# Optimization experiments

Hardware: AMD Instinct MI355X
Metric: run time of the kernel (lower is better)

Reference implementation:

```python
import jax, jax.numpy as jnp
import numpy as np

B, N, C = 64, 512, 1280


def setup_inputs() -> dict:
    key = jax.random.key(0)
    ks = jax.random.split(key, 10)
    scale = 0.02
    x = jax.random.normal(ks[0], (B, N, C), dtype=jnp.float32)
    Mask = jax.random.randint(ks[1], (B, N, N), 0, 2, dtype=jnp.int32)
    Wq = jax.random.normal(ks[2], (C, C), dtype=jnp.float32) * scale
    bq = jnp.zeros((C,), dtype=jnp.float32)
    Wk = jax.random.normal(ks[3], (C, C), dtype=jnp.float32) * scale
    bk = jnp.zeros((C,), dtype=jnp.float32)
    Wv = jax.random.normal(ks[4], (C, C), dtype=jnp.float32) * scale
    bv = jnp.zeros((C,), dtype=jnp.float32)
    Wr = jax.random.normal(ks[5], (C, C), dtype=jnp.float32) * scale
    br = jnp.zeros((C,), dtype=jnp.float32)
    return {"x": x, "Mask": Mask, "Wq": Wq, "bq": bq, "Wk": Wk, "bk": bk,
            "Wv": Wv, "bv": bv, "Wr": Wr, "br": br}


def reference(x, Mask, Wq, bq, Wk, bk, Wv, bv, Wr, br):
    # q, k, v: [B, N, C]
    q = x @ Wq + bq
    k = x @ Wk + bk
    v = x @ Wv + bv
    # scores[b, n, m] = q[b, n] . k[b, m]  -> [B, N, N]
    scores = jnp.einsum('bnc,bmc->bnm', q, k)
    # masked_fill BEFORE the scale divide, as in the original module
    scores = jnp.where(Mask == 0, jnp.float32(-1e20), scores)
    attn = jax.nn.softmax(scores / jnp.sqrt(jnp.float32(C)), axis=-1)
    # original: (V^T @ attn).permute -> out[b, n, c] = sum_m v[b, m, c] * attn[b, m, n]
    att_feat = jnp.einsum('bmc,bmn->bnc', v, attn)
    return att_feat @ Wr + br
```

## Files before the change

kernel.cpp:

```cpp
#include <hip/hip_runtime.h>
#include <hip/hip_bf16.h>

#define DI __device__ __forceinline__

typedef __attribute__((ext_vector_type(8))) short short8;
typedef __attribute__((ext_vector_type(4))) float f32x4;

DI unsigned short f2bf(float f) {
    union { float f; unsigned int u; } v; v.f = f;
    unsigned int r = v.u + 0x7FFFu + ((v.u >> 16) & 1u);
    return (unsigned short)(r >> 16);
}
DI float bf2f(unsigned short h) {
    union { unsigned int u; float f; } v; v.u = ((unsigned int)h) << 16;
    return v.f;
}

#define GLD16(g, l) __builtin_amdgcn_global_load_lds( \
    (const __attribute__((address_space(1))) void*)(g), \
    (__attribute__((address_space(3))) void*)(l), 16, 0, 0)

template<int EPI, int QKV>
__global__ __launch_bounds__(512, 2) void gemm256(
    const unsigned short* __restrict__ A, const unsigned short* __restrict__ Bt,
    void* __restrict__ Cout, const float* __restrict__ bias,
    const float* __restrict__ bias1, const float* __restrict__ bias2,
    const int* __restrict__ mask, int K, int lda, int ldb, int ldc,
    long sA, long sB, long sC, long sM, float scale)
{
    __shared__ unsigned short lds[65536];

    const unsigned gx = gridDim.x, gy = gridDim.y;
    unsigned lin = blockIdx.x + gx * (blockIdx.y + gy * blockIdx.z);
    const unsigned nwg = gx * gy * gridDim.z;
    lin = (lin & 7u) * (nwg >> 3) + (lin >> 3);
    int tn = lin % gx;
    const int tm = (lin / gx) % gy;
    const int z = lin / (gx * gy);

    if (QKV) {
        const int g = tn / 5; tn -= g * 5;
        Bt += (size_t)g * sB;
        Cout = (void*)((unsigned short*)Cout + (size_t)g * sC);
        if (g == 1) bias = bias1; else if (g == 2) bias = bias2;
    }

    const unsigned short* Ab = A + (long)z * sA + (size_t)(tm * 256) * lda;
    const unsigned short* Bb = Bt + (QKV ? 0 : (long)z * sB) + (size_t)(tn * 256) * ldb;

    const int tid = threadIdx.x, wave = tid >> 6, l = tid & 63;
    const int wr = wave >> 2, wc = wave & 3;

    const int srow = wave * 32 + (l >> 2);
    const int schunk = ((l & 3) ^ ((l >> 3) & 3)) * 8;
    const unsigned short* agS = Ab + (size_t)srow * lda + schunk;
    const unsigned short* bgS = Bb + (size_t)srow * ldb + schunk;
    unsigned short* ldsA0 = &lds[wave * 1024];
    unsigned short* ldsB0 = &lds[8192 + wave * 1024];

    const int rl = l & 15;
    const int cl8 = ((l >> 4) ^ ((l >> 1) & 3)) * 8;
    const int aoff = (wr * 128 + rl) * 32 + cl8;
    const int boff = 8192 + (wc * 64 + rl) * 32 + cl8;

#define REGOFF(buf, h) (((buf) * 2 + (h)) * 16384)
#define SA(t, h, buf) { const unsigned short* g_ = agS + (size_t)((t) * 64 + (h) * 32); \
    GLD16(g_, ldsA0 + REGOFF(buf, h)); \
    GLD16(g_ + (size_t)16 * lda, ldsA0 + REGOFF(buf, h) + 512); }
#define SB(t, h, buf) { const unsigned short* g_ = bgS + (size_t)((t) * 64 + (h) * 32); \
    GLD16(g_, ldsB0 + REGOFF(buf, h)); \
    GLD16(g_ + (size_t)16 * ldb, ldsB0 + REGOFF(buf, h) + 512); }

    f32x4 acc[8][4] = {};

#define PHASE(buf, h, STG, VMW) { \
    short8 af[8], bfv[4]; \
    _Pragma("unroll") for (int i = 0; i < 4; ++i) \
        af[i] = *(const short8*)&lds[REGOFF(buf, h) + aoff + i * 512]; \
    _Pragma("unroll") for (int n = 0; n < 4; ++n) \
        bfv[n] = *(const short8*)&lds[REGOFF(buf, h) + boff + n * 512]; \
    _Pragma("unroll") for (int i = 4; i < 8; ++i) \
        af[i] = *(const short8*)&lds[REGOFF(buf, h) + aoff + i * 512]; \
    STG; \
    asm volatile("s_waitcnt lgkmcnt(4)" ::: "memory"); \
    __builtin_amdgcn_sched_barrier(0); \
    __builtin_amdgcn_s_setprio(1); \
    _Pragma("unroll") for (int i = 0; i < 4; ++i) \
        _Pragma("unroll") for (int n = 0; n < 4; ++n) \
            acc[i][n] = __builtin_amdgcn_mfma_f32_16x16x32_bf16( \
                af[i], bfv[n], acc[i][n], 0, 0, 0); \
    asm volatile("s_waitcnt lgkmcnt(0)" ::: "memory"); \
    __builtin_amdgcn_sched_barrier(0); \
    _Pragma("unroll") for (int i = 4; i < 8; ++i) \
        _Pragma("unroll") for (int n = 0; n < 4; ++n) \
            acc[i][n] = __builtin_amdgcn_mfma_f32_16x16x32_bf16( \
                af[i], bfv[n], acc[i][n], 0, 0, 0); \
    __builtin_amdgcn_s_setprio(0); \
    asm volatile("s_waitcnt " VMW ::: "memory"); \
    __builtin_amdgcn_s_barrier(); \
  }

    SA(0, 0, 0); SB(0, 0, 0); SA(0, 1, 0); SB(0, 1, 0); SA(1, 0, 1); SB(1, 0, 1);
    asm volatile("s_waitcnt vmcnt(8)" ::: "memory");
    __builtin_amdgcn_s_barrier();

    const int NI = K >> 7;
    for (int j = 0; j < NI - 1; ++j) {
        const int t = 2 * j;
        PHASE(0, 0, SA(t + 1, 1, 1) SB(t + 1, 1, 1), "vmcnt(8)")
        PHASE(0, 1, SA(t + 2, 0, 0) SB(t + 2, 0, 0), "vmcnt(8)")
        PHASE(1, 0, SA(t + 2, 1, 0) SB(t + 2, 1, 0), "vmcnt(8)")
        PHASE(1, 1, SA(t + 3, 0, 1) SB(t + 3, 0, 1), "vmcnt(8)")
    }
    {
        const int t = 2 * (NI - 1);
        PHASE(0, 0, SA(t + 1, 1, 1) SB(t + 1, 1, 1), "vmcnt(8)")
        PHASE(0, 1, ((void)0),                       "vmcnt(4)")
        PHASE(1, 0, ((void)0),                       "vmcnt(0)")
        PHASE(1, 1, ((void)0),                       "vmcnt(0)")
    }
#undef PHASE
#undef SA
#undef SB
#undef REGOFF

    const long cb = QKV ? 0 : (long)z * sC;
    const int row0 = tm * 256 + wr * 128 + (l >> 4) * 4;
    const int col0 = tn * 256 + wc * 64 + rl;

    if (EPI == 0) {
        float b4[4];
        #pragma unroll
        for (int n = 0; n < 4; ++n) b4[n] = bias[col0 + n * 16];
        unsigned short* gout = (unsigned short*)Cout;
        #pragma unroll
        for (int half = 0; half < 2; ++half) {
            if (wr == half) {
                #pragma unroll
                for (int mi = 0; mi < 8; ++mi)
                    #pragma unroll
                    for (int n = 0; n < 4; ++n)
                        #pragma unroll
                        for (int r = 0; r < 4; ++r) {
                            const int lr = mi * 16 + ((l >> 4) << 2) + r;
                            const int lc = wc * 64 + n * 16 + rl;
                            lds[lr * 264 + lc] = f2bf(acc[mi][n][r] + b4[n]);
                        }
            }
            __syncthreads();
            const long rbase = (long)(tm * 256 + half * 128);
            #pragma unroll
            for (int rr = 0; rr < 8; ++rr) {
                const int row = rr * 16 + (tid >> 5);
                const int ch = tid & 31;
                short8 vv = *(const short8*)&lds[row * 264 + ch * 8];
                __builtin_nontemporal_store(vv,
                    (short8*)&gout[(rbase + row) * (size_t)ldc + tn * 256 + ch * 8]);
            }
            __syncthreads();
        }
    } else {
        #pragma unroll
        for (int mi = 0; mi < 8; ++mi) {
            #pragma unroll
            for (int n = 0; n < 4; ++n) {
                #pragma unroll
                for (int r = 0; r < 4; ++r) {
                    const int row = row0 + mi * 16 + r;
                    const int col = col0 + n * 16;
                    float v = acc[mi][n][r];
                    if (EPI == 3) v += bias[col];
                    if (EPI == 1) {
                        v *= scale;
                        if (mask[(long)z * sM + (long)row * ldc + col] == 0)
                            v = -1e20f * scale;
                    }
                    if (EPI == 3)
                        __builtin_nontemporal_store(v, &((float*)Cout)[cb + (long)row * ldc + col]);
                    else
                        ((unsigned short*)Cout)[cb + (long)row * ldc + col] = f2bf(v);
                }
            }
        }
    }
}

__global__ void transpose_w(const float* __restrict__ Wq, const float* __restrict__ Wk,
                            const float* __restrict__ Wv, const float* __restrict__ Wr,
                            unsigned short* __restrict__ Wt)
{
    const float* W = blockIdx.z == 0 ? Wq : blockIdx.z == 1 ? Wk : blockIdx.z == 2 ? Wv : Wr;
    unsigned short* dst = Wt + (size_t)blockIdx.z * 1280 * 1280;
    __shared__ float T[64][65];
    const int j0 = blockIdx.x * 64, k0 = blockIdx.y * 64;
    const int tid = threadIdx.x;
    for (int it = 0; it < 16; ++it) {
        int idx = it * 256 + tid;
        int r = idx >> 6, c = idx & 63;
        T[r][c] = W[(size_t)(k0 + r) * 1280 + j0 + c];
    }
    __syncthreads();
    for (int it = 0; it < 16; ++it) {
        int idx = it * 256 + tid;
        int r = idx >> 6, c = idx & 63;
        dst[(size_t)(j0 + r) * 1280 + k0 + c] = f2bf(T[c][r]);
    }
}

__global__ void cast_x(const float* __restrict__ x, unsigned short* __restrict__ xb, long n)
{
    long i = ((long)blockIdx.x * 256 + threadIdx.x) * 8;
    if (i + 8 > n) return;
    const float4* p = (const float4*)(x + i);
    float4 a = p[0], b = p[1];
    unsigned short o[8] = { f2bf(a.x), f2bf(a.y), f2bf(a.z), f2bf(a.w),
                            f2bf(b.x), f2bf(b.y), f2bf(b.z), f2bf(b.w) };
    *(short8*)(xb + i) = *(short8*)o;
}

#define SMS 514
__global__ void softmax_t(const unsigned short* __restrict__ S, unsigned short* __restrict__ Pt)
{
    __shared__ unsigned short T[64 * SMS];
    __shared__ float rmax[64], rinv[64];
    const int b = blockIdx.y, mb = blockIdx.x * 64;
    const int tid = threadIdx.x, lane = tid & 63, wave = tid >> 6;
    const unsigned short* src = S + ((size_t)b * 512 + mb) * 512;

    for (int rr = 0; rr < 16; ++rr) {
        int r = rr * 4 + wave;
        const unsigned int* s = (const unsigned int*)(src + (size_t)r * 512);
        unsigned int* t = (unsigned int*)&T[r * SMS];
        #pragma unroll
        for (int j = 0; j < 4; ++j) t[lane + j * 64] = s[lane + j * 64];
    }
    __syncthreads();

    {
        int r = tid >> 2, q = tid & 3;
        const unsigned short* row = &T[r * SMS + q * 128];
        float mx = -3.0e38f;
        for (int i = 0; i < 128; ++i) mx = fmaxf(mx, bf2f(row[i]));
        mx = fmaxf(mx, __shfl_xor(mx, 1));
        mx = fmaxf(mx, __shfl_xor(mx, 2));
        float s = 0.f;
        for (int i = 0; i < 128; ++i) s += expf(bf2f(row[i]) - mx);
        s += __shfl_xor(s, 1);
        s += __shfl_xor(s, 2);
        if (q == 0) { rmax[r] = mx; rinv[r] = 1.0f / s; }
    }
    __syncthreads();

    {
        int m = tid & 63, nq = tid >> 6;
        float mxm = rmax[m], rim = rinv[m];
        unsigned short* dst = Pt + (size_t)b * 512 * 512 + mb + m;
        for (int it = 0; it < 128; ++it) {
            int n = it * 4 + nq;
            float v = expf(bf2f(T[m * SMS + n]) - mxm) * rim;
            dst[(size_t)n * 512] = f2bf(v);
        }
    }
}

__global__ void transpose_v(const unsigned short* __restrict__ V, unsigned short* __restrict__ Vt)
{
    __shared__ unsigned short T[64][65];
    const int b = blockIdx.z;
    const int c0 = blockIdx.x * 64, m0 = blockIdx.y * 64;
    const int tid = threadIdx.x;
    const unsigned short* src = V + ((size_t)b * 512 + m0) * 1280 + c0;
    for (int it = 0; it < 16; ++it) {
        int idx = it * 256 + tid;
        int r = idx >> 6, c = idx & 63;
        T[r][c] = src[(size_t)r * 1280 + c];
    }
    __syncthreads();
    unsigned short* dst = Vt + ((size_t)b * 1280 + c0) * 512 + m0;
    for (int it = 0; it < 16; ++it) {
        int idx = it * 256 + tid;
        int r = idx >> 6, c = idx & 63;
        dst[(size_t)r * 512 + c] = T[c][r];
    }
}

extern "C" void kernel_launch(void* const* d_in, const int* in_sizes, int n_in,
                              void* d_out, int out_size, void* d_ws, size_t ws_size,
                              hipStream_t stream)
{
    const float* x   = (const float*)d_in[0];
    const int*  Mask = (const int*)d_in[1];
    const float* Wq  = (const float*)d_in[2];
    const float* bq  = (const float*)d_in[3];
    const float* Wk  = (const float*)d_in[4];
    const float* bk  = (const float*)d_in[5];
    const float* Wv  = (const float*)d_in[6];
    const float* bv  = (const float*)d_in[7];
    const float* Wr  = (const float*)d_in[8];
    const float* br  = (const float*)d_in[9];

    constexpr int N = 512, C = 1280;
    constexpr long MN = 32768;

    char* ws = (char*)d_ws;
    unsigned short* xb = (unsigned short*)ws;
    unsigned short* Wt = (unsigned short*)(ws + 83886080);
    unsigned short* Q  = (unsigned short*)(ws + 83886080 + 13107200);
    unsigned short* Km = Q + 41943040;
    unsigned short* V  = Km + 41943040;
    unsigned short* Sp = V + 41943040;
    unsigned short* Pt = Sp + 16777216;
    unsigned short* Vt = Q;
    unsigned short* att = xb;

    const float scale = 0.02795084971874737f;

    transpose_w<<<dim3(20, 20, 4), 256, 0, stream>>>(Wq, Wk, Wv, Wr, Wt);
    cast_x<<<dim3(20480), 256, 0, stream>>>(x, xb, MN * C);

    gemm256<0, 1><<<dim3(15, 128, 1), 512, 0, stream>>>(xb, Wt, (void*)Q, bq, bk, bv,
        nullptr, C, C, C, C, 0, 1638400L, 41943040L, 0, 0.f);

    gemm256<1, 0><<<dim3(2, 2, 64), 512, 0, stream>>>(Q, Km, (void*)Sp, nullptr, nullptr, nullptr,
        Mask, C, C, C, N, (long)N * C, (long)N * C, (long)N * N, (long)N * N, scale);

    softmax_t<<<dim3(8, 64), 256, 0, stream>>>(Sp, Pt);

    transpose_v<<<dim3(20, 8, 64), 256, 0, stream>>>(V, Vt);

    gemm256<2, 0><<<dim3(5, 2, 64), 512, 0, stream>>>(Pt, Vt, (void*)att, nullptr, nullptr, nullptr,
        nullptr, N, N, N, C, (long)N * N, (long)C * N, (long)N * C, 0, 0.f);

    gemm256<3, 0><<<dim3(5, 128, 1), 512, 0, stream>>>(att, Wt + 3 * 1638400, d_out, br, nullptr, nullptr,
        nullptr, C, C, C, C, 0, 0, 0, 0, 0.f);
}
```

Before: 698.8 us.

## Use 4-wave 256x256 GEMM blocks with 128x128 per-wave tiles and 4-slot pipeline

The GEMM kernel now runs with 256 threads (4 waves) instead of 512, so each wave computes a 128x128 sub-tile with 8x8 accumulator fragments. Global-to-LDS staging becomes a 4-slot ring of 32-wide K slices with deeper vmcnt waits, and the epilogues are adapted to the wider per-wave column span. The goal is higher MFMA-to-LDS-read ratio per wave and fewer barriers per K step. In exchange, accumulator register use doubles and occupancy drops to one block per CU, which risks spills and less latency hiding.

```diff
diff --git a/kernel.cpp b/kernel.cpp
--- a/kernel.cpp
+++ b/kernel.cpp
@@ -21,7 +21,7 @@
     (__attribute__((address_space(3))) void*)(l), 16, 0, 0)
 
 template<int EPI, int QKV>
-__global__ __launch_bounds__(512, 2) void gemm256(
+__global__ __launch_bounds__(256, 1) void gemm256(
     const unsigned short* __restrict__ A, const unsigned short* __restrict__ Bt,
     void* __restrict__ Cout, const float* __restrict__ bias,
     const float* __restrict__ bias1, const float* __restrict__ bias2,
@@ -49,50 +49,53 @@
     const unsigned short* Bb = Bt + (QKV ? 0 : (long)z * sB) + (size_t)(tn * 256) * ldb;
 
     const int tid = threadIdx.x, wave = tid >> 6, l = tid & 63;
-    const int wr = wave >> 2, wc = wave & 3;
-
-    const int srow = wave * 32 + (l >> 2);
+    const int wr = wave >> 1, wc = wave & 1;
+
     const int schunk = ((l & 3) ^ ((l >> 3) & 3)) * 8;
-    const unsigned short* agS = Ab + (size_t)srow * lda + schunk;
-    const unsigned short* bgS = Bb + (size_t)srow * ldb + schunk;
-    unsigned short* ldsA0 = &lds[wave * 1024];
-    unsigned short* ldsB0 = &lds[8192 + wave * 1024];
+    const unsigned short* agS = Ab + (size_t)(wave * 16 + (l >> 2)) * lda + schunk;
+    const unsigned short* bgS = Bb + (size_t)(wave * 16 + (l >> 2)) * ldb + schunk;
+    unsigned short* ldsA = &lds[wave * 512];
+    unsigned short* ldsB = &lds[8192 + wave * 512];
 
     const int rl = l & 15;
     const int cl8 = ((l >> 4) ^ ((l >> 1) & 3)) * 8;
     const int aoff = (wr * 128 + rl) * 32 + cl8;
-    const int boff = 8192 + (wc * 64 + rl) * 32 + cl8;
-
-#define REGOFF(buf, h) (((buf) * 2 + (h)) * 16384)
-#define SA(t, h, buf) { const unsigned short* g_ = agS + (size_t)((t) * 64 + (h) * 32); \
-    GLD16(g_, ldsA0 + REGOFF(buf, h)); \
-    GLD16(g_ + (size_t)16 * lda, ldsA0 + REGOFF(buf, h) + 512); }
-#define SB(t, h, buf) { const unsigned short* g_ = bgS + (size_t)((t) * 64 + (h) * 32); \
-    GLD16(g_, ldsB0 + REGOFF(buf, h)); \
-    GLD16(g_ + (size_t)16 * ldb, ldsB0 + REGOFF(buf, h) + 512); }
-
-    f32x4 acc[8][4] = {};
-
-#define PHASE(buf, h, STG, VMW) { \
-    short8 af[8], bfv[4]; \
+    const int boff = 8192 + (wc * 128 + rl) * 32 + cl8;
+
+#define SLOTOFF(s) ((s) * 16384)
+#define SA4(t, s) { const unsigned short* g_ = agS + (size_t)(t) * 32; \
+    GLD16(g_,                      ldsA + SLOTOFF(s)); \
+    GLD16(g_ + (size_t)64 * lda,   ldsA + SLOTOFF(s) + 2048); \
+    GLD16(g_ + (size_t)128 * lda,  ldsA + SLOTOFF(s) + 4096); \
+    GLD16(g_ + (size_t)192 * lda,  ldsA + SLOTOFF(s) + 6144); }
+#define SB4(t, s) { const unsigned short* g_ = bgS + (size_t)(t) * 32; \
+    GLD16(g_,                      ldsB + SLOTOFF(s)); \
+    GLD16(g_ + (size_t)64 * ldb,   ldsB + SLOTOFF(s) + 2048); \
+    GLD16(g_ + (size_t)128 * ldb,  ldsB + SLOTOFF(s) + 4096); \
+    GLD16(g_ + (size_t)192 * ldb,  ldsB + SLOTOFF(s) + 6144); }
+
+    f32x4 acc[8][8] = {};
+
+#define PHASE(s, STG, VMW) { \
+    short8 af[8], bfv[8]; \
     _Pragma("unroll") for (int i = 0; i < 4; ++i) \
-        af[i] = *(const short8*)&lds[REGOFF(buf, h) + aoff + i * 512]; \
-    _Pragma("unroll") for (int n = 0; n < 4; ++n) \
-        bfv[n] = *(const short8*)&lds[REGOFF(buf, h) + boff + n * 512]; \
+        af[i] = *(const short8*)&lds[SLOTOFF(s) + aoff + i * 512]; \
+    _Pragma("unroll") for (int n = 0; n < 8; ++n) \
+        bfv[n] = *(const short8*)&lds[SLOTOFF(s) + boff + n * 512]; \
     _Pragma("unroll") for (int i = 4; i < 8; ++i) \
-        af[i] = *(const short8*)&lds[REGOFF(buf, h) + aoff + i * 512]; \
+        af[i] = *(const short8*)&lds[SLOTOFF(s) + aoff + i * 512]; \
     STG; \
     asm volatile("s_waitcnt lgkmcnt(4)" ::: "memory"); \
     __builtin_amdgcn_sched_barrier(0); \
     __builtin_amdgcn_s_setprio(1); \
     _Pragma("unroll") for (int i = 0; i < 4; ++i) \
-        _Pragma("unroll") for (int n = 0; n < 4; ++n) \
+        _Pragma("unroll") for (int n = 0; n < 8; ++n) \
             acc[i][n] = __builtin_amdgcn_mfma_f32_16x16x32_bf16( \
                 af[i], bfv[n], acc[i][n], 0, 0, 0); \
     asm volatile("s_waitcnt lgkmcnt(0)" ::: "memory"); \
     __builtin_amdgcn_sched_barrier(0); \
     _Pragma("unroll") for (int i = 4; i < 8; ++i) \
-        _Pragma("unroll") for (int n = 0; n < 4; ++n) \
+        _Pragma("unroll") for (int n = 0; n < 8; ++n) \
             acc[i][n] = __builtin_amdgcn_mfma_f32_16x16x32_bf16( \
                 af[i], bfv[n], acc[i][n], 0, 0, 0); \
     __builtin_amdgcn_s_setprio(0); \
@@ -100,38 +103,38 @@
     __builtin_amdgcn_s_barrier(); \
   }
 
-    SA(0, 0, 0); SB(0, 0, 0); SA(0, 1, 0); SB(0, 1, 0); SA(1, 0, 1); SB(1, 0, 1);
-    asm volatile("s_waitcnt vmcnt(8)" ::: "memory");
+    SA4(0, 0) SB4(0, 0) SA4(1, 1) SB4(1, 1) SA4(2, 2) SB4(2, 2)
+    asm volatile("s_waitcnt vmcnt(16)" ::: "memory");
     __builtin_amdgcn_s_barrier();
 
-    const int NI = K >> 7;
-    for (int j = 0; j < NI - 1; ++j) {
-        const int t = 2 * j;
-        PHASE(0, 0, SA(t + 1, 1, 1) SB(t + 1, 1, 1), "vmcnt(8)")
-        PHASE(0, 1, SA(t + 2, 0, 0) SB(t + 2, 0, 0), "vmcnt(8)")
-        PHASE(1, 0, SA(t + 2, 1, 0) SB(t + 2, 1, 0), "vmcnt(8)")
-        PHASE(1, 1, SA(t + 3, 0, 1) SB(t + 3, 0, 1), "vmcnt(8)")
+    const int NR = K >> 5;
+    for (int j = 0; j < (NR >> 2) - 1; ++j) {
+        const int t = 4 * j;
+        PHASE(0, SA4(t + 3, 3) SB4(t + 3, 3), "vmcnt(16)")
+        PHASE(1, SA4(t + 4, 0) SB4(t + 4, 0), "vmcnt(16)")
+        PHASE(2, SA4(t + 5, 1) SB4(t + 5, 1), "vmcnt(16)")
+        PHASE(3, SA4(t + 6, 2) SB4(t + 6, 2), "vmcnt(16)")
     }
     {
-        const int t = 2 * (NI - 1);
-        PHASE(0, 0, SA(t + 1, 1, 1) SB(t + 1, 1, 1), "vmcnt(8)")
-        PHASE(0, 1, ((void)0),                       "vmcnt(4)")
-        PHASE(1, 0, ((void)0),                       "vmcnt(0)")
-        PHASE(1, 1, ((void)0),                       "vmcnt(0)")
+        const int t = NR - 4;
+        PHASE(0, SA4(t + 3, 3) SB4(t + 3, 3), "vmcnt(16)")
+        PHASE(1, ((void)0),                   "vmcnt(8)")
+        PHASE(2, ((void)0),                   "vmcnt(0)")
+        PHASE(3, ((void)0),                   "vmcnt(0)")
     }
 #undef PHASE
-#undef SA
-#undef SB
-#undef REGOFF
+#undef SA4
+#undef SB4
+#undef SLOTOFF
 
     const long cb = QKV ? 0 : (long)z * sC;
     const int row0 = tm * 256 + wr * 128 + (l >> 4) * 4;
-    const int col0 = tn * 256 + wc * 64 + rl;
+    const int col0 = tn * 256 + wc * 128 + rl;
 
     if (EPI == 0) {
-        float b4[4];
+        float b8[8];
         #pragma unroll
-        for (int n = 0; n < 4; ++n) b4[n] = bias[col0 + n * 16];
+        for (int n = 0; n < 8; ++n) b8[n] = bias[col0 + n * 16];
         unsigned short* gout = (unsigned short*)Cout;
         #pragma unroll
         for (int half = 0; half < 2; ++half) {
@@ -139,19 +142,19 @@
                 #pragma unroll
                 for (int mi = 0; mi < 8; ++mi)
                     #pragma unroll
-                    for (int n = 0; n < 4; ++n)
+                    for (int n = 0; n < 8; ++n)
                         #pragma unroll
                         for (int r = 0; r < 4; ++r) {
                             const int lr = mi * 16 + ((l >> 4) << 2) + r;
-                            const int lc = wc * 64 + n * 16 + rl;
-                            lds[lr * 264 + lc] = f2bf(acc[mi][n][r] + b4[n]);
+                            const int lc = wc * 128 + n * 16 + rl;
+                            lds[lr * 264 + lc] = f2bf(acc[mi][n][r] + b8[n]);
                         }
             }
             __syncthreads();
             const long rbase = (long)(tm * 256 + half * 128);
             #pragma unroll
-            for (int rr = 0; rr < 8; ++rr) {
-                const int row = rr * 16 + (tid >> 5);
+            for (int rr = 0; rr < 16; ++rr) {
+                const int row = rr * 8 + (tid >> 5);
                 const int ch = tid & 31;
                 short8 vv = *(const short8*)&lds[row * 264 + ch * 8];
                 __builtin_nontemporal_store(vv,
@@ -163,7 +166,7 @@
         #pragma unroll
         for (int mi = 0; mi < 8; ++mi) {
             #pragma unroll
-            for (int n = 0; n < 4; ++n) {
+            for (int n = 0; n < 8; ++n) {
                 #pragma unroll
                 for (int r = 0; r < 4; ++r) {
                     const int row = row0 + mi * 16 + r;
@@ -318,19 +321,19 @@
     transpose_w<<<dim3(20, 20, 4), 256, 0, stream>>>(Wq, Wk, Wv, Wr, Wt);
     cast_x<<<dim3(20480), 256, 0, stream>>>(x, xb, MN * C);
 
-    gemm256<0, 1><<<dim3(15, 128, 1), 512, 0, stream>>>(xb, Wt, (void*)Q, bq, bk, bv,
+    gemm256<0, 1><<<dim3(15, 128, 1), 256, 0, stream>>>(xb, Wt, (void*)Q, bq, bk, bv,
         nullptr, C, C, C, C, 0, 1638400L, 41943040L, 0, 0.f);
 
-    gemm256<1, 0><<<dim3(2, 2, 64), 512, 0, stream>>>(Q, Km, (void*)Sp, nullptr, nullptr, nullptr,
+    gemm256<1, 0><<<dim3(2, 2, 64), 256, 0, stream>>>(Q, Km, (void*)Sp, nullptr, nullptr, nullptr,
         Mask, C, C, C, N, (long)N * C, (long)N * C, (long)N * N, (long)N * N, scale);
 
     softmax_t<<<dim3(8, 64), 256, 0, stream>>>(Sp, Pt);
 
     transpose_v<<<dim3(20, 8, 64), 256, 0, stream>>>(V, Vt);
 
-    gemm256<2, 0><<<dim3(5, 2, 64), 512, 0, stream>>>(Pt, Vt, (void*)att, nullptr, nullptr, nullptr,
+    gemm256<2, 0><<<dim3(5, 2, 64), 256, 0, stream>>>(Pt, Vt, (void*)att, nullptr, nullptr, nullptr,
         nullptr, N, N, N, C, (long)N * N, (long)C * N, (long)N * C, 0, 0.f);
 
-    gemm256<3, 0><<<dim3(5, 128, 1), 512, 0, stream>>>(att, Wt + 3 * 1638400, d_out, br, nullptr, nullptr,
+    gemm256<3, 0><<<dim3(5, 128, 1), 256, 0, stream>>>(att, Wt + 3 * 1638400, d_out, br, nullptr, nullptr,
         nullptr, C, C, C, C, 0, 0, 0, 0, 0.f);
 }
```

Result: slower. 764.8 us (+9.5%).
